# Performance work log

Hardware: AMD Instinct MI355X
Metric: run time of the kernel (lower is better)

## Reference

```python
import jax, jax.numpy as jnp
import numpy as np

SIGMAS = [1.0, 1.5, 2.0, 3.0]


def _gauss1d(sigma):
    ks = int(4 * sigma + 1)
    if ks % 2 == 0:
        ks += 1
    x = np.arange(ks, dtype=np.float32) - ks // 2
    k = np.exp(-0.5 * x ** 2 / sigma ** 2)
    return jnp.asarray(k / k.sum(), dtype=jnp.float32)


def _conv_axis(x, k1d, axis):
    """1D conv along spatial axis (2=z,3=y,4=x) of NCDHW tensor, 'same' padding."""
    K = k1d.shape[0]
    kshape = [1, 1, 1, 1, 1]
    kshape[axis] = K
    ker = k1d.reshape(kshape)  # OIDHW, O=I=1
    pad = [(0, 0), (0, 0), (0, 0)]
    pad[axis - 2] = (K // 2, K // 2)
    return jax.lax.conv_general_dilated(
        x, ker, window_strides=(1, 1, 1), padding=pad,
        dimension_numbers=('NCDHW', 'OIDHW', 'NCDHW'))


def _gauss_smooth(x, sigma):
    k = _gauss1d(sigma)
    x = _conv_axis(x, k, 2)
    x = _conv_axis(x, k, 3)
    x = _conv_axis(x, k, 4)
    return x


def setup_inputs() -> dict:
    key = jax.random.key(0)
    raw = jax.random.normal(key, (1, 1, 192, 192, 192), dtype=jnp.float32)
    return {"raw": raw}


def reference(raw) -> jnp.ndarray:
    grad_k = jnp.asarray([-0.5, 0.0, 0.5], dtype=jnp.float32)
    d2_k = jnp.asarray([1.0, -2.0, 1.0], dtype=jnp.float32)

    ch0 = raw
    g1_0 = _gauss_smooth(raw, 1.0)
    g1_5 = _gauss_smooth(raw, 1.5)
    ch1 = g1_0 - g1_5
    g2_0 = _gauss_smooth(raw, 2.0)
    g3_0 = _gauss_smooth(raw, 3.0)
    ch2 = g2_0 - g3_0

    smooth = g1_0
    gz = _conv_axis(smooth, grad_k, 2)
    gy = _conv_axis(smooth, grad_k, 3)
    gx = _conv_axis(smooth, grad_k, 4)
    hzz = _conv_axis(smooth, d2_k, 2)
    hyy = _conv_axis(smooth, d2_k, 3)
    hxx = _conv_axis(smooth, d2_k, 4)

    ch3 = hzz + hyy + hxx                                    # Laplacian
    ch4 = jnp.sqrt(gz ** 2 + gy ** 2 + gx ** 2 + 1e-08)     # gradient magnitude
    ch5 = jnp.clip(jnp.abs(gy) / (jnp.abs(gx) + 0.001), 0.0, 20.0)

    features = jnp.concatenate([ch0, ch1, ch2, ch3, ch4, ch5], axis=1)  # [B,6,D,H,W]
    mean = jnp.mean(features, axis=(2, 3, 4), keepdims=True)
    # torch .std() is unbiased (ddof=1)
    std = jnp.std(features, axis=(2, 3, 4), keepdims=True, ddof=1)
    return (features - mean) / (std + 1e-08)
```

## Files before the change

kernel.cpp:

```cpp
#include <hip/hip_runtime.h>
#include <hip/hip_fp16.h>
#include <cmath>

#define DIM 192
#define V (DIM * DIM * DIM)
#define V4 (V / 4)
#define ROW4 (DIM / 4)
#define SLAB4 (ROW4 * DIM)
#define NSLOT 64
#define ZB 4
#define TY 16
#define YXB (DIM * (DIM / TY))

struct ZW { float w10[13], w15[13], w20[13], w30[13]; };
struct W2 { float wA[13], wB[13]; };

__device__ inline void fma4(float4& a, float w, const float4& v) {
    a.x += w * v.x; a.y += w * v.y; a.z += w * v.z; a.w += w * v.w;
}

__device__ inline uint2 pack_h4(float4 v) {
    __half2 lo = __floats2half2_rn(v.x, v.y);
    __half2 hi = __floats2half2_rn(v.z, v.w);
    uint2 r;
    r.x = *(unsigned int*)&lo;
    r.y = *(unsigned int*)&hi;
    return r;
}
__device__ inline float4 unpack_h4(uint2 p) {
    __half2 lo = *(__half2*)&p.x;
    __half2 hi = *(__half2*)&p.y;
    float2 a = __half22float2(lo), b = __half22float2(hi);
    return make_float4(a.x, a.y, b.x, b.y);
}
__device__ inline float4 ld4(const float4* p, int i) { return p[i]; }
__device__ inline float4 ld4(const uint2*  p, int i) { return unpack_h4(p[i]); }

__device__ inline void block_reduce_slot2(float s, float s2,
                                          double* slots0, double* slots1) {
    __shared__ float ws[4], ws2[4];
    __syncthreads();
    for (int m = 1; m < 64; m <<= 1) {
        s  += __shfl_xor(s,  m, 64);
        s2 += __shfl_xor(s2, m, 64);
    }
    int wid = threadIdx.x >> 6, lane = threadIdx.x & 63;
    if (lane == 0) { ws[wid] = s; ws2[wid] = s2; }
    __syncthreads();
    if (threadIdx.x == 0) {
        int slot = blockIdx.x & (NSLOT - 1);
        atomicAdd(&slots0[slot], (double)(ws[0] + ws[1] + ws[2] + ws[3]));
        atomicAdd(&slots1[slot], (double)(ws2[0] + ws2[1] + ws2[2] + ws2[3]));
    }
}

__global__ __launch_bounds__(256) void zpass4(const float4* __restrict__ raw,
        float4* __restrict__ g10z, uint2* __restrict__ g15z,
        uint2* __restrict__ g20z, uint2* __restrict__ g30z,
        ZW zw, double* __restrict__ slots) {
    int tid = blockIdx.x * 256 + threadIdx.x;
    int x4 = tid % ROW4;
    int y  = (tid / ROW4) % DIM;
    int zg = tid / (ROW4 * DIM);
    int z0 = zg * ZB;
    int base = y * ROW4 + x4;
    float4 a10[ZB], a15[ZB], a20[ZB], a30[ZB];
#pragma unroll
    for (int k = 0; k < ZB; ++k) {
        a10[k] = make_float4(0,0,0,0); a15[k] = make_float4(0,0,0,0);
        a20[k] = make_float4(0,0,0,0); a30[k] = make_float4(0,0,0,0);
    }
    float s = 0.f, s2 = 0.f;
#pragma unroll
    for (int j = 0; j < ZB + 12; ++j) {
        int zz = z0 + j - 6;
        if (zz >= 0 && zz < DIM) {
            float4 v = raw[zz * SLAB4 + base];
#pragma unroll
            for (int k = 0; k < ZB; ++k) {
                int w = j - k;
                if (w >= 0 && w <= 12) {
                    fma4(a10[k], zw.w10[w], v);
                    fma4(a15[k], zw.w15[w], v);
                    fma4(a20[k], zw.w20[w], v);
                    fma4(a30[k], zw.w30[w], v);
                }
            }
            if (j >= 6 && j < 6 + ZB) {
                s  += v.x + v.y + v.z + v.w;
                s2 += v.x*v.x + v.y*v.y + v.z*v.z + v.w*v.w;
            }
        }
    }
#pragma unroll
    for (int k = 0; k < ZB; ++k) {
        int idx = (z0 + k) * SLAB4 + base;
        g10z[idx] = a10[k];
        g15z[idx] = pack_h4(a15[k]);
        g20z[idx] = pack_h4(a20[k]);
        g30z[idx] = pack_h4(a30[k]);
    }
    block_reduce_slot2(s, s2, slots + 0 * NSLOT, slots + 1 * NSLOT);
}

template <int KYA, int KYB, int KXA, int KXB, bool WRITE_G, bool OUT_H,
          typename TA, typename TB>
__device__ void yx_tile(int tile, const TA* __restrict__ inA,
        const TB* __restrict__ inB, float4* __restrict__ outG,
        float4* __restrict__ outCf, uint2* __restrict__ outCh,
        float4* yA4, float4* yB4,
        const W2& wy, const W2& wx, double* s0, double* s1) {
    constexpr int NF4 = TY * ROW4;
    constexpr int HXA = KXA / 2, HXB = KXB / 2;
    constexpr int WQA = (HXA + 3) / 4;
    constexpr int WQB = (HXB + 3) / 4;
    int z  = tile / (DIM / TY);
    int y0 = (tile % (DIM / TY)) * TY;
    const int slab = z * SLAB4;
    for (int e = threadIdx.x; e < NF4; e += 256) {
        int r  = e / ROW4;
        int x4 = e % ROW4;
        int y  = y0 + r;
        float4 a = {0,0,0,0}, b = {0,0,0,0};
#pragma unroll
        for (int t = 0; t < KYA; ++t) {
            int yy = y + t - KYA / 2;
            if (yy >= 0 && yy < DIM) fma4(a, wy.wA[t], ld4(inA, slab + yy * ROW4 + x4));
        }
#pragma unroll
        for (int t = 0; t < KYB; ++t) {
            int yy = y + t - KYB / 2;
            if (yy >= 0 && yy < DIM) fma4(b, wy.wB[t], ld4(inB, slab + yy * ROW4 + x4));
        }
        yA4[e] = a;
        yB4[e] = b;
    }
    __syncthreads();
    float s = 0.f, s2 = 0.f;
    for (int e = threadIdx.x; e < NF4; e += 256) {
        int r = e / ROW4, x4 = e % ROW4;
        const float4* rowA = yA4 + r * ROW4;
        const float4* rowB = yB4 + r * ROW4;
        float wa[4 * (2 * WQA + 1)], wb[4 * (2 * WQB + 1)];
#pragma unroll
        for (int q = -WQA; q <= WQA; ++q) {
            float4 v = ((unsigned)(x4 + q) < (unsigned)ROW4) ? rowA[x4 + q]
                                                             : make_float4(0,0,0,0);
            int b0 = 4 * (q + WQA);
            wa[b0] = v.x; wa[b0 + 1] = v.y; wa[b0 + 2] = v.z; wa[b0 + 3] = v.w;
        }
#pragma unroll
        for (int q = -WQB; q <= WQB; ++q) {
            float4 v = ((unsigned)(x4 + q) < (unsigned)ROW4) ? rowB[x4 + q]
                                                             : make_float4(0,0,0,0);
            int b0 = 4 * (q + WQB);
            wb[b0] = v.x; wb[b0 + 1] = v.y; wb[b0 + 2] = v.z; wb[b0 + 3] = v.w;
        }
        float g[4], cv[4];
#pragma unroll
        for (int j = 0; j < 4; ++j) {
            float ca = 0.f, cb = 0.f;
#pragma unroll
            for (int t = 0; t < KXA; ++t) ca += wx.wA[t] * wa[4 * WQA + j + t - HXA];
#pragma unroll
            for (int t = 0; t < KXB; ++t) cb += wx.wB[t] * wb[4 * WQB + j + t - HXB];
            g[j] = ca;
            cv[j] = ca - cb;
            s += cv[j]; s2 += cv[j] * cv[j];
        }
        int gi = slab + (y0 + r) * ROW4 + x4;
        if constexpr (WRITE_G) outG[gi] = make_float4(g[0], g[1], g[2], g[3]);
        if constexpr (OUT_H)   outCh[gi] = pack_h4(make_float4(cv[0], cv[1], cv[2], cv[3]));
        else                   outCf[gi] = make_float4(cv[0], cv[1], cv[2], cv[3]);
    }
    block_reduce_slot2(s, s2, s0, s1);
}

__global__ __launch_bounds__(256) void yx_both(
        const float4* __restrict__ g10z, const uint2* __restrict__ g15z,
        const uint2* __restrict__ g20z, const uint2* __restrict__ g30z,
        float4* __restrict__ o0, float4* __restrict__ o1, float4* __restrict__ o2,
        uint2* __restrict__ ch1h, uint2* __restrict__ ch2h, int useH,
        W2 wyA, W2 wxA, W2 wyB, W2 wxB, double* __restrict__ slots) {
    __shared__ float4 yA4[TY * ROW4], yB4[TY * ROW4];
    int bid = blockIdx.x;
    if (bid < YXB) {
        if (useH)
            yx_tile<5, 7, 5, 7, true, true>(bid, g10z, g15z, o0, (float4*)nullptr,
                ch1h, yA4, yB4, wyA, wxA, slots + 2 * NSLOT, slots + 3 * NSLOT);
        else
            yx_tile<5, 7, 5, 7, true, false>(bid, g10z, g15z, o0, o1,
                (uint2*)nullptr, yA4, yB4, wyA, wxA, slots + 2 * NSLOT, slots + 3 * NSLOT);
    } else {
        bid -= YXB;
        if (useH)
            yx_tile<9, 13, 9, 13, false, true>(bid, g20z, g30z, (float4*)nullptr,
                (float4*)nullptr, ch2h, yA4, yB4, wyB, wxB,
                slots + 4 * NSLOT, slots + 5 * NSLOT);
        else
            yx_tile<9, 13, 9, 13, false, false>(bid, g20z, g30z, (float4*)nullptr,
                o2, (uint2*)nullptr, yA4, yB4, wyB, wxB,
                slots + 4 * NSLOT, slots + 5 * NSLOT);
    }
}

__device__ inline void deriv_point(const float4* g4, const float* g, int i,
                                   float o3[4], float o4[4], float o5[4]) {
    int x4 = i % ROW4;
    int y  = (i / ROW4) % DIM;
    int z  = i / SLAB4;
    const float4 zero = {0,0,0,0};
    float4 c  = g4[i];
    float4 zm = (z > 0)       ? g4[i - SLAB4] : zero;
    float4 zp = (z < DIM - 1) ? g4[i + SLAB4] : zero;
    float4 ym = (y > 0)       ? g4[i - ROW4]  : zero;
    float4 yp = (y < DIM - 1) ? g4[i + ROW4]  : zero;
    float lf = (x4 > 0)        ? g[4 * i - 1] : 0.f;
    float rt = (x4 < ROW4 - 1) ? g[4 * i + 4] : 0.f;
    float xm[4] = { lf, c.x, c.y, c.z };
    float xp[4] = { c.y, c.z, c.w, rt };
    float cc[4] = { c.x, c.y, c.z, c.w };
    float zmv[4] = { zm.x, zm.y, zm.z, zm.w };
    float zpv[4] = { zp.x, zp.y, zp.z, zp.w };
    float ymv[4] = { ym.x, ym.y, ym.z, ym.w };
    float ypv[4] = { yp.x, yp.y, yp.z, yp.w };
#pragma unroll
    for (int j = 0; j < 4; ++j) {
        float gx = 0.5f * (xp[j] - xm[j]);
        float gy = 0.5f * (ypv[j] - ymv[j]);
        float gz = 0.5f * (zpv[j] - zmv[j]);
        o3[j] = xm[j] + xp[j] + ymv[j] + ypv[j] + zmv[j] + zpv[j] - 6.f * cc[j];
        o4[j] = sqrtf(gx * gx + gy * gy + gz * gz + 1e-8f);
        o5[j] = fminf(fabsf(gy) / (fabsf(gx) + 1e-3f), 20.f);
    }
}

__global__ __launch_bounds__(256) void deriv_stats(const float4* __restrict__ g4,
        const float* __restrict__ g, double* __restrict__ slots) {
    int i = blockIdx.x * 256 + threadIdx.x;
    float o3[4], o4[4], o5[4];
    deriv_point(g4, g, i, o3, o4, o5);
    float s3 = 0, q3 = 0, s4 = 0, q4 = 0, s5 = 0, q5 = 0;
#pragma unroll
    for (int j = 0; j < 4; ++j) {
        s3 += o3[j]; q3 += o3[j] * o3[j];
        s4 += o4[j]; q4 += o4[j] * o4[j];
        s5 += o5[j]; q5 += o5[j] * o5[j];
    }
    block_reduce_slot2(s3, q3, slots + 6 * NSLOT,  slots + 7 * NSLOT);
    block_reduce_slot2(s4, q4, slots + 8 * NSLOT,  slots + 9 * NSLOT);
    block_reduce_slot2(s5, q5, slots + 10 * NSLOT, slots + 11 * NSLOT);
}

__global__ void finalize_sums(const double* __restrict__ slots,
                              double* __restrict__ finals) {
    int w = threadIdx.x >> 6, lane = threadIdx.x & 63;
    for (int t = w; t < 12; t += 4) {
        double s = slots[t * NSLOT + lane];
        for (int m = 1; m < 64; m <<= 1) s += __shfl_xor(s, m, 64);
        if (lane == 0) finals[t] = s;
    }
}

__device__ inline void mean_inv(const double* finals, int c, float& m, float& inv) {
    double s = finals[2 * c], s2 = finals[2 * c + 1];
    double mean = s / (double)V;
    double var  = (s2 - s * s / (double)V) / (double)(V - 1);
    m   = (float)mean;
    inv = (float)(1.0 / (sqrt(var) + 1e-8));
}

__global__ __launch_bounds__(256) void norm_deriv(const float4* __restrict__ g4,
        const float* __restrict__ g, float4* __restrict__ c3,
        float4* __restrict__ c4o, float4* __restrict__ c5,
        const double* __restrict__ finals) {
    int i = blockIdx.x * 256 + threadIdx.x;
    float o3[4], o4[4], o5[4];
    deriv_point(g4, g, i, o3, o4, o5);
    float m3, i3, m4, i4, m5, i5;
    mean_inv(finals, 3, m3, i3);
    mean_inv(finals, 4, m4, i4);
    mean_inv(finals, 5, m5, i5);
    c3[i]  = make_float4((o3[0]-m3)*i3, (o3[1]-m3)*i3, (o3[2]-m3)*i3, (o3[3]-m3)*i3);
    c4o[i] = make_float4((o4[0]-m4)*i4, (o4[1]-m4)*i4, (o4[2]-m4)*i4, (o4[3]-m4)*i4);
    c5[i]  = make_float4((o5[0]-m5)*i5, (o5[1]-m5)*i5, (o5[2]-m5)*i5, (o5[3]-m5)*i5);
}

__global__ __launch_bounds__(256) void norm_abc(const float4* __restrict__ raw,
        const uint2* __restrict__ ch1h, const uint2* __restrict__ ch2h,
        float4* __restrict__ out, const double* __restrict__ finals, int useH) {
    int i = blockIdx.x * 256 + threadIdx.x;
    int c = i / V4;
    int ii = i - c * V4;
    float m, inv;
    mean_inv(finals, c, m, inv);
    float4 v;
    if (c == 0)     v = raw[ii];
    else if (useH)  v = unpack_h4((c == 1 ? ch1h : ch2h)[ii]);
    else            v = out[(size_t)c * V4 + ii];
    v.x = (v.x - m) * inv;
    v.y = (v.y - m) * inv;
    v.z = (v.z - m) * inv;
    v.w = (v.w - m) * inv;
    out[(size_t)c * V4 + ii] = v;
}

static void gauss_w(double sigma, float* w13, int center) {
    int ks = (int)(4.0 * sigma + 1.0);
    if (ks % 2 == 0) ks++;
    double tmp[13], sum = 0.0;
    for (int i = 0; i < ks; ++i) {
        double x = (double)(i - ks / 2);
        tmp[i] = exp(-0.5 * x * x / (sigma * sigma));
        sum += tmp[i];
    }
    for (int i = 0; i < 13; ++i) w13[i] = 0.f;
    int h = ks / 2;
    for (int i = 0; i < ks; ++i) w13[center + (i - h)] = (float)(tmp[i] / sum);
}

extern "C" void kernel_launch(void* const* d_in, const int* in_sizes, int n_in,
                              void* d_out, int out_size, void* d_ws, size_t ws_size,
                              hipStream_t stream) {
    const float* raw = (const float*)d_in[0];
    float* out = (float*)d_out;
    float* o[6];
    for (int c = 0; c < 6; ++c) o[c] = out + (size_t)c * V;
    double* slots  = (double*)d_ws;
    double* finals = slots + 12 * NSLOT;

    size_t stage_off = 8192;
    size_t stage_need = stage_off + 2 * (size_t)V4 * sizeof(uint2);
    int useH = (ws_size >= stage_need) ? 1 : 0;
    uint2* ch1h = (uint2*)((char*)d_ws + stage_off);
    uint2* ch2h = ch1h + V4;

    hipMemsetAsync(d_ws, 0, (12 * NSLOT + 12) * sizeof(double), stream);

    ZW zw;
    gauss_w(1.0, zw.w10, 6); gauss_w(1.5, zw.w15, 6);
    gauss_w(2.0, zw.w20, 6); gauss_w(3.0, zw.w30, 6);
    W2 wyA; gauss_w(1.0, wyA.wA, 2);  gauss_w(1.5, wyA.wB, 3);
    W2 wxA; gauss_w(1.0, wxA.wA, 2);  gauss_w(1.5, wxA.wB, 3);
    W2 wyB; gauss_w(2.0, wyB.wA, 4);  gauss_w(3.0, wyB.wB, 6);
    W2 wxB; gauss_w(2.0, wxB.wA, 4);  gauss_w(3.0, wxB.wB, 6);

    const float4* raw4 = (const float4*)raw;
    dim3 blk(256);
    int g4blocks = V4 / 256;
    int zblocks  = V4 / (ZB * 256);

    float4* g10z = (float4*)o[5];
    uint2*  g15z = (uint2*)o[3];
    uint2*  g20z = (uint2*)o[3] + V4;
    uint2*  g30z = (uint2*)o[4];

    zpass4<<<zblocks, blk, 0, stream>>>(raw4, g10z, g15z, g20z, g30z, zw, slots);
    yx_both<<<2 * YXB, blk, 0, stream>>>(g10z, g15z, g20z, g30z,
        (float4*)o[0], (float4*)o[1], (float4*)o[2], ch1h, ch2h, useH,
        wyA, wxA, wyB, wxB, slots);
    deriv_stats<<<g4blocks, blk, 0, stream>>>((const float4*)o[0], o[0], slots);
    finalize_sums<<<1, 256, 0, stream>>>(slots, finals);
    norm_deriv<<<g4blocks, blk, 0, stream>>>((const float4*)o[0], o[0],
        (float4*)o[3], (float4*)o[4], (float4*)o[5], finals);
    norm_abc<<<(3 * V4) / 256, blk, 0, stream>>>(raw4, ch1h, ch2h,
        (float4*)out, finals, useH);
}
```

Before: 202.5 us.

## Stage y-halo rows in LDS, swizzle blocks across XCDs, fold stats finalize into consumers

The yx pass now loads each tile's input rows plus the y-halo into shared memory once, instead of re-reading global memory for every vertical tap. Block indices are remapped so consecutive tiles go to the same XCD, which is meant to improve L2 locality. The separate finalize_sums launch is removed: every block of the norm kernels reduces the 64 slots itself. This saves one launch, but each block repeats the slot reads and a shuffle reduction, and the larger shared-memory footprint may lower occupancy.

```diff
diff --git a/kernel.cpp b/kernel.cpp
--- a/kernel.cpp
+++ b/kernel.cpp
@@ -19,6 +19,11 @@
     a.x += w * v.x; a.y += w * v.y; a.z += w * v.z; a.w += w * v.w;
 }
 
+__device__ inline int xcd_swz() {
+    int b = blockIdx.x;
+    return (b & 7) * (gridDim.x >> 3) + (b >> 3);
+}
+
 __device__ inline uint2 pack_h4(float4 v) {
     __half2 lo = __floats2half2_rn(v.x, v.y);
     __half2 hi = __floats2half2_rn(v.z, v.w);
@@ -35,6 +40,8 @@
 }
 __device__ inline float4 ld4(const float4* p, int i) { return p[i]; }
 __device__ inline float4 ld4(const uint2*  p, int i) { return unpack_h4(p[i]); }
+__device__ inline void   st4(float4* p, int i, float4 v) { p[i] = v; }
+__device__ inline void   st4(uint2*  p, int i, float4 v) { p[i] = pack_h4(v); }
 
 __device__ inline void block_reduce_slot2(float s, float s2,
                                           double* slots0, double* slots1) {
@@ -54,11 +61,29 @@
     }
 }
 
+__device__ inline void fold_slots(const double* __restrict__ slots, int base,
+                                  int n, double* fin) {
+    int w = threadIdx.x >> 6, lane = threadIdx.x & 63;
+    for (int t = base + w; t < base + n; t += 4) {
+        double s = slots[t * NSLOT + lane];
+        for (int m = 1; m < 64; m <<= 1) s += __shfl_xor(s, m, 64);
+        if (lane == 0) fin[t - base] = s;
+    }
+    __syncthreads();
+}
+
+__device__ inline void mean_inv2(double s, double s2, float& m, float& inv) {
+    double mean = s / (double)V;
+    double var  = (s2 - s * s / (double)V) / (double)(V - 1);
+    m   = (float)mean;
+    inv = (float)(1.0 / (sqrt(var) + 1e-8));
+}
+
 __global__ __launch_bounds__(256) void zpass4(const float4* __restrict__ raw,
         float4* __restrict__ g10z, uint2* __restrict__ g15z,
         uint2* __restrict__ g20z, uint2* __restrict__ g30z,
         ZW zw, double* __restrict__ slots) {
-    int tid = blockIdx.x * 256 + threadIdx.x;
+    int tid = xcd_swz() * 256 + threadIdx.x;
     int x4 = tid % ROW4;
     int y  = (tid / ROW4) % DIM;
     int zg = tid / (ROW4 * DIM);
@@ -108,30 +133,42 @@
 __device__ void yx_tile(int tile, const TA* __restrict__ inA,
         const TB* __restrict__ inB, float4* __restrict__ outG,
         float4* __restrict__ outCf, uint2* __restrict__ outCh,
-        float4* yA4, float4* yB4,
+        char* stage, float4* yA4, float4* yB4,
         const W2& wy, const W2& wx, double* s0, double* s1) {
     constexpr int NF4 = TY * ROW4;
+    constexpr int HYA = KYA / 2, HYB = KYB / 2;
+    constexpr int SR  = TY + 2 * HYB;
     constexpr int HXA = KXA / 2, HXB = KXB / 2;
     constexpr int WQA = (HXA + 3) / 4;
     constexpr int WQB = (HXB + 3) / 4;
+    TA* sA = (TA*)stage;
+    TB* sB = (TB*)(stage + sizeof(TA) * SR * ROW4);
     int z  = tile / (DIM / TY);
     int y0 = (tile % (DIM / TY)) * TY;
     const int slab = z * SLAB4;
+    for (int e = threadIdx.x; e < SR * ROW4; e += 256) {
+        int r  = e / ROW4;
+        int x4 = e % ROW4;
+        int yy = y0 - HYB + r;
+        bool ok = (yy >= 0 && yy < DIM);
+        int gi = slab + yy * ROW4 + x4;
+        if (ok) { sA[e] = inA[gi]; sB[e] = inB[gi]; }
+        else {
+            st4(sA, e, make_float4(0,0,0,0));
+            st4(sB, e, make_float4(0,0,0,0));
+        }
+    }
+    __syncthreads();
     for (int e = threadIdx.x; e < NF4; e += 256) {
         int r  = e / ROW4;
         int x4 = e % ROW4;
-        int y  = y0 + r;
         float4 a = {0,0,0,0}, b = {0,0,0,0};
 #pragma unroll
-        for (int t = 0; t < KYA; ++t) {
-            int yy = y + t - KYA / 2;
-            if (yy >= 0 && yy < DIM) fma4(a, wy.wA[t], ld4(inA, slab + yy * ROW4 + x4));
-        }
-#pragma unroll
-        for (int t = 0; t < KYB; ++t) {
-            int yy = y + t - KYB / 2;
-            if (yy >= 0 && yy < DIM) fma4(b, wy.wB[t], ld4(inB, slab + yy * ROW4 + x4));
-        }
+        for (int t = 0; t < KYA; ++t)
+            fma4(a, wy.wA[t], ld4(sA, (r + t + HYB - HYA) * ROW4 + x4));
+#pragma unroll
+        for (int t = 0; t < KYB; ++t)
+            fma4(b, wy.wB[t], ld4(sB, (r + t) * ROW4 + x4));
         yA4[e] = a;
         yB4[e] = b;
     }
@@ -176,30 +213,34 @@
     block_reduce_slot2(s, s2, s0, s1);
 }
 
+#define STAGE_BYTES 25344
+
 __global__ __launch_bounds__(256) void yx_both(
         const float4* __restrict__ g10z, const uint2* __restrict__ g15z,
         const uint2* __restrict__ g20z, const uint2* __restrict__ g30z,
         float4* __restrict__ o0, float4* __restrict__ o1, float4* __restrict__ o2,
         uint2* __restrict__ ch1h, uint2* __restrict__ ch2h, int useH,
         W2 wyA, W2 wxA, W2 wyB, W2 wxB, double* __restrict__ slots) {
+    __shared__ __align__(16) char stage[STAGE_BYTES];
     __shared__ float4 yA4[TY * ROW4], yB4[TY * ROW4];
-    int bid = blockIdx.x;
+    int bid = xcd_swz();
     if (bid < YXB) {
         if (useH)
             yx_tile<5, 7, 5, 7, true, true>(bid, g10z, g15z, o0, (float4*)nullptr,
-                ch1h, yA4, yB4, wyA, wxA, slots + 2 * NSLOT, slots + 3 * NSLOT);
+                ch1h, stage, yA4, yB4, wyA, wxA, slots + 2 * NSLOT, slots + 3 * NSLOT);
         else
             yx_tile<5, 7, 5, 7, true, false>(bid, g10z, g15z, o0, o1,
-                (uint2*)nullptr, yA4, yB4, wyA, wxA, slots + 2 * NSLOT, slots + 3 * NSLOT);
+                (uint2*)nullptr, stage, yA4, yB4, wyA, wxA,
+                slots + 2 * NSLOT, slots + 3 * NSLOT);
     } else {
         bid -= YXB;
         if (useH)
             yx_tile<9, 13, 9, 13, false, true>(bid, g20z, g30z, (float4*)nullptr,
-                (float4*)nullptr, ch2h, yA4, yB4, wyB, wxB,
+                (float4*)nullptr, ch2h, stage, yA4, yB4, wyB, wxB,
                 slots + 4 * NSLOT, slots + 5 * NSLOT);
         else
             yx_tile<9, 13, 9, 13, false, false>(bid, g20z, g30z, (float4*)nullptr,
-                o2, (uint2*)nullptr, yA4, yB4, wyB, wxB,
+                o2, (uint2*)nullptr, stage, yA4, yB4, wyB, wxB,
                 slots + 4 * NSLOT, slots + 5 * NSLOT);
     }
 }
@@ -237,7 +278,7 @@
 
 __global__ __launch_bounds__(256) void deriv_stats(const float4* __restrict__ g4,
         const float* __restrict__ g, double* __restrict__ slots) {
-    int i = blockIdx.x * 256 + threadIdx.x;
+    int i = xcd_swz() * 256 + threadIdx.x;
     float o3[4], o4[4], o5[4];
     deriv_point(g4, g, i, o3, o4, o5);
     float s3 = 0, q3 = 0, s4 = 0, q4 = 0, s5 = 0, q5 = 0;
@@ -252,35 +293,19 @@
     block_reduce_slot2(s5, q5, slots + 10 * NSLOT, slots + 11 * NSLOT);
 }
 
-__global__ void finalize_sums(const double* __restrict__ slots,
-                              double* __restrict__ finals) {
-    int w = threadIdx.x >> 6, lane = threadIdx.x & 63;
-    for (int t = w; t < 12; t += 4) {
-        double s = slots[t * NSLOT + lane];
-        for (int m = 1; m < 64; m <<= 1) s += __shfl_xor(s, m, 64);
-        if (lane == 0) finals[t] = s;
-    }
-}
-
-__device__ inline void mean_inv(const double* finals, int c, float& m, float& inv) {
-    double s = finals[2 * c], s2 = finals[2 * c + 1];
-    double mean = s / (double)V;
-    double var  = (s2 - s * s / (double)V) / (double)(V - 1);
-    m   = (float)mean;
-    inv = (float)(1.0 / (sqrt(var) + 1e-8));
-}
-
 __global__ __launch_bounds__(256) void norm_deriv(const float4* __restrict__ g4,
         const float* __restrict__ g, float4* __restrict__ c3,
         float4* __restrict__ c4o, float4* __restrict__ c5,
-        const double* __restrict__ finals) {
-    int i = blockIdx.x * 256 + threadIdx.x;
+        const double* __restrict__ slots) {
+    __shared__ double fin[6];
+    fold_slots(slots, 6, 6, fin);
+    int i = xcd_swz() * 256 + threadIdx.x;
     float o3[4], o4[4], o5[4];
     deriv_point(g4, g, i, o3, o4, o5);
     float m3, i3, m4, i4, m5, i5;
-    mean_inv(finals, 3, m3, i3);
-    mean_inv(finals, 4, m4, i4);
-    mean_inv(finals, 5, m5, i5);
+    mean_inv2(fin[0], fin[1], m3, i3);
+    mean_inv2(fin[2], fin[3], m4, i4);
+    mean_inv2(fin[4], fin[5], m5, i5);
     c3[i]  = make_float4((o3[0]-m3)*i3, (o3[1]-m3)*i3, (o3[2]-m3)*i3, (o3[3]-m3)*i3);
     c4o[i] = make_float4((o4[0]-m4)*i4, (o4[1]-m4)*i4, (o4[2]-m4)*i4, (o4[3]-m4)*i4);
     c5[i]  = make_float4((o5[0]-m5)*i5, (o5[1]-m5)*i5, (o5[2]-m5)*i5, (o5[3]-m5)*i5);
@@ -288,12 +313,14 @@
 
 __global__ __launch_bounds__(256) void norm_abc(const float4* __restrict__ raw,
         const uint2* __restrict__ ch1h, const uint2* __restrict__ ch2h,
-        float4* __restrict__ out, const double* __restrict__ finals, int useH) {
+        float4* __restrict__ out, const double* __restrict__ slots, int useH) {
+    __shared__ double fin[6];
+    fold_slots(slots, 0, 6, fin);
     int i = blockIdx.x * 256 + threadIdx.x;
     int c = i / V4;
     int ii = i - c * V4;
     float m, inv;
-    mean_inv(finals, c, m, inv);
+    mean_inv2(fin[2 * c], fin[2 * c + 1], m, inv);
     float4 v;
     if (c == 0)     v = raw[ii];
     else if (useH)  v = unpack_h4((c == 1 ? ch1h : ch2h)[ii]);
@@ -326,8 +353,7 @@
     float* out = (float*)d_out;
     float* o[6];
     for (int c = 0; c < 6; ++c) o[c] = out + (size_t)c * V;
-    double* slots  = (double*)d_ws;
-    double* finals = slots + 12 * NSLOT;
+    double* slots = (double*)d_ws;
 
     size_t stage_off = 8192;
     size_t stage_need = stage_off + 2 * (size_t)V4 * sizeof(uint2);
@@ -335,7 +361,7 @@
     uint2* ch1h = (uint2*)((char*)d_ws + stage_off);
     uint2* ch2h = ch1h + V4;
 
-    hipMemsetAsync(d_ws, 0, (12 * NSLOT + 12) * sizeof(double), stream);
+    hipMemsetAsync(d_ws, 0, 12 * NSLOT * sizeof(double), stream);
 
     ZW zw;
     gauss_w(1.0, zw.w10, 6); gauss_w(1.5, zw.w15, 6);
@@ -360,9 +386,8 @@
         (float4*)o[0], (float4*)o[1], (float4*)o[2], ch1h, ch2h, useH,
         wyA, wxA, wyB, wxB, slots);
     deriv_stats<<<g4blocks, blk, 0, stream>>>((const float4*)o[0], o[0], slots);
-    finalize_sums<<<1, 256, 0, stream>>>(slots, finals);
     norm_deriv<<<g4blocks, blk, 0, stream>>>((const float4*)o[0], o[0],
-        (float4*)o[3], (float4*)o[4], (float4*)o[5], finals);
+        (float4*)o[3], (float4*)o[4], (float4*)o[5], slots);
     norm_abc<<<(3 * V4) / 256, blk, 0, stream>>>(raw4, ch1h, ch2h,
-        (float4*)out, finals, useH);
-}
+        (float4*)out, slots, useH);
+}
```

Measured after the change: 185.0 us. -8.6%, faster.
